# Kernel tuning notes

Measured on AMD Instinct MI355X. Metric: run time of the kernel, lower is better.

Reference implementation:

```python
import jax, jax.numpy as jnp
from jax import lax
import numpy as np

FEA = 256
NHEADS = 8
GROUPS = 32
SCALE = 1.0 / np.sqrt(FEA // NHEADS)  # 1/sqrt(qkv_dim//nheads)


def conv2d(x, w, b=None, pad=0, groups=1):
    out = lax.conv_general_dilated(
        x, w, (1, 1), [(pad, pad), (pad, pad)],
        dimension_numbers=("NCHW", "OIHW", "NCHW"),
        feature_group_count=groups)
    return out if b is None else out + b[None, :, None, None]


def group_norm(x, w, b, groups=GROUPS, eps=1e-5):
    B, C, H, W = x.shape
    xg = x.reshape(B, groups, C // groups, H, W)
    m = xg.mean(axis=(2, 3, 4), keepdims=True)
    v = xg.var(axis=(2, 3, 4), keepdims=True)
    xg = (xg - m) * lax.rsqrt(v + eps)
    return xg.reshape(B, C, H, W) * w[None, :, None, None] + b[None, :, None, None]


def l2norm(x, eps=1e-12):  # F.normalize over channel dim
    n = jnp.sqrt(jnp.sum(x * x, axis=1, keepdims=True))
    return x / jnp.maximum(n, eps)


def attn_op(q, k, v):
    b, c, xf, yf = q.shape
    sp = lambda t: t.reshape(b, NHEADS, c // NHEADS, xf * yf)
    q, k, v = sp(q), sp(k), sp(v)
    sim = jnp.einsum("bhjn,bhkn->bhjk", q, k) * SCALE  # channel attention, [b,h,c/h,c/h]
    sim = jax.nn.softmax(sim, axis=-1)
    out = jnp.einsum("bhjk,bhkn->bhjn", sim, v)
    return out.reshape(b, c, xf, yf)


def freqca(x, gn_w, gn_b, dw_w, pw_w, pw_b, ao_w, ao_b, f1_w, f2_w, f3_w, f3_b):
    H, W = x.shape[-2:]
    x = group_norm(x, gn_w, gn_b)
    qkv = conv2d(conv2d(x, dw_w, pad=1, groups=FEA), pw_w, pw_b)  # depthwise 3x3 then 1x1 -> 3*qkv_dim
    q, k, v = jnp.split(qkv, 3, axis=1)
    q, k, v = l2norm(q), l2norm(k), l2norm(v)
    qf = jnp.fft.rfft2(q, axes=(-2, -1), norm="ortho")
    kf = jnp.fft.rfft2(k, axes=(-2, -1), norm="ortho")
    vf = jnp.fft.rfft2(v, axes=(-2, -1), norm="ortho")
    amp = attn_op(jnp.abs(qf), jnp.abs(kf), jnp.abs(vf))
    phas = attn_op(jnp.angle(qf), jnp.angle(kf), jnp.angle(vf))
    out_c = amp * jnp.cos(phas) + 1j * (amp * jnp.sin(phas))  # torch.polar
    out = jnp.fft.irfft2(out_c, s=(H, W), axes=(-2, -1), norm="ortho")
    attn = conv2d(out, ao_w, ao_b) + x  # attn_res is Identity (fea_dim == dim_out)
    h = jax.nn.silu(conv2d(attn, f1_w, pad=1))
    h = conv2d(h, f2_w, pad=1)
    h = conv2d(h, f3_w, f3_b)
    return h + attn  # DropPath in eval mode = identity


def setup_inputs() -> dict:
    key = jax.random.key(0)
    ks = jax.random.split(key, 12)
    B, C, H, W = 8, FEA, 128, 128
    s = 0.02
    return {
        "x": jax.random.normal(ks[0], (B, C, H, W), jnp.float32),
        "gn_w": jnp.ones((C,), jnp.float32),
        "gn_b": jnp.zeros((C,), jnp.float32),
        "dw_w": jax.random.normal(ks[1], (C, 1, 3, 3), jnp.float32) * s,
        "pw_w": jax.random.normal(ks[2], (3 * C, C, 1, 1), jnp.float32) * s,
        "pw_b": jnp.zeros((3 * C,), jnp.float32),
        "ao_w": jax.random.normal(ks[3], (C, C, 1, 1), jnp.float32) * s,
        "ao_b": jnp.zeros((C,), jnp.float32),
        "f1_w": jax.random.normal(ks[4], (2 * C, C, 3, 3), jnp.float32) * s,
        "f2_w": jax.random.normal(ks[5], (C, 2 * C, 3, 3), jnp.float32) * s,
        "f3_w": jax.random.normal(ks[6], (C, C, 1, 1), jnp.float32) * s,
        "f3_b": jnp.zeros((C,), jnp.float32),
    }


def reference(x, gn_w, gn_b, dw_w, pw_w, pw_b, ao_w, ao_b, f1_w, f2_w, f3_w, f3_b):
    return freqca(x, gn_w, gn_b, dw_w, pw_w, pw_b, ao_w, ao_b, f1_w, f2_w, f3_w, f3_b)
```

## Files before the change

kernel.cpp:

```cpp
#include <hip/hip_runtime.h>
#include <hip/hip_bf16.h>
#include <math.h>


#define TWO_PI_D 6.283185307179586476925286766559
#define ATTN_SCALE 0.17677669529663687f

typedef __attribute__((ext_vector_type(8))) short short8;
typedef __attribute__((ext_vector_type(4))) short short4v;
typedef __attribute__((ext_vector_type(4))) float f32x4;
typedef _Float16 half8v __attribute__((ext_vector_type(8)));

__device__ inline short f2bf(float f) {
    __hip_bfloat16 h = __float2bfloat16(f);
    return *reinterpret_cast<short*>(&h);
}
__device__ inline unsigned short h_bits(_Float16 h) {
    union { _Float16 h; unsigned short u; } c; c.h = h; return c.u;
}

__global__ __launch_bounds__(256) void groupnorm_kernel(
    const float* __restrict__ x, const float* __restrict__ gw,
    const float* __restrict__ gb, float* __restrict__ out, int b0)
{
    int t = threadIdx.x;
    int lb = blockIdx.x >> 5;
    int g  = blockIdx.x & 31;
    size_t src = ((size_t)(b0 + lb) * 32 + g) * 131072;
    size_t dst = (size_t)blockIdx.x * 131072;
    const float* xp = x + src;
    double s = 0.0, ss = 0.0;
    for (int i = t; i < 131072; i += 256) { double v = xp[i]; s += v; ss += v*v; }
    __shared__ double rs[256], rss[256];
    rs[t] = s; rss[t] = ss;
    __syncthreads();
    for (int k = 128; k > 0; k >>= 1) {
        if (t < k) { rs[t] += rs[t+k]; rss[t] += rss[t+k]; }
        __syncthreads();
    }
    __shared__ float smean, sinv;
    if (t == 0) {
        double mean = rs[0] * (1.0/131072.0);
        double var  = rss[0] * (1.0/131072.0) - mean*mean;
        smean = (float)mean;
        sinv  = (float)(1.0 / sqrt(var + 1e-5));
    }
    __syncthreads();
    float mean = smean, inv = sinv;
    for (int i = t; i < 131072; i += 256) {
        int c = (g << 3) + (i >> 14);
        out[dst + i] = (xp[i] - mean) * inv * gw[c] + gb[c];
    }
}

__global__ __launch_bounds__(256) void dwconv_kernel(
    const float* __restrict__ in, const float* __restrict__ w, float* __restrict__ out)
{
    int t = threadIdx.x;
    int bc = blockIdx.x >> 6;
    int y  = ((blockIdx.x & 63) << 1) + (t >> 7);
    int x  = t & 127;
    int c  = bc & 255;
    const float* wp = w + c*9;
    const float* ip = in + ((size_t)bc << 14);
    float acc = 0.f;
    #pragma unroll
    for (int dy = 0; dy < 3; dy++) {
        int yy = y + dy - 1;
        if (yy < 0 || yy > 127) continue;
        const float* row = ip + (yy << 7);
        #pragma unroll
        for (int dx = 0; dx < 3; dx++) {
            int xx = x + dx - 1;
            if (xx >= 0 && xx <= 127) acc += wp[dy*3+dx] * row[xx];
        }
    }
    out[((size_t)bc << 14) + (y << 7) + x] = acc;
}

__global__ __launch_bounds__(256) void wcvtpw_kernel(
    const float* __restrict__ w, _Float16* __restrict__ whi,
    _Float16* __restrict__ wlo, int total)
{
    int i = blockIdx.x * 256 + threadIdx.x;
    if (i >= total) return;
    float v = w[i];
    _Float16 h = (_Float16)v;
    _Float16 l = (_Float16)(v - (float)h);
    whi[i] = h; wlo[i] = l;
}

__global__ __launch_bounds__(256) void convpw_kernel(
    const float* __restrict__ in, const _Float16* __restrict__ whi,
    const _Float16* __restrict__ wlo, const float* __restrict__ bias,
    float* __restrict__ out)
{
    int y      = blockIdx.x;
    int coBase = blockIdx.y << 7;
    int lb     = blockIdx.z;
    int t = threadIdx.x;
    int lane = t & 63;
    int wave = t >> 6;
    int wm = (wave >> 1) << 6;
    int wn = (wave & 1) << 6;
    int lr = lane & 15;
    int kg = (lane >> 4) << 3;

    __shared__ _Float16 Ah[128][40], Al[128][40];
    __shared__ _Float16 Bh[128][40], Bl[128][40];

    f32x4 acc[4][4];
    #pragma unroll
    for (int i = 0; i < 4; i++)
        #pragma unroll
        for (int j = 0; j < 4; j++) acc[i][j] = (f32x4){0.f, 0.f, 0.f, 0.f};

    const float* inrow = in + (((size_t)lb * 256) << 14) + (y << 7);
    for (int ci0 = 0; ci0 < 256; ci0 += 32) {
        __syncthreads();
        #pragma unroll
        for (int u = 0; u < 2; u++) {
            int ii = t + (u << 8);
            int co = ii >> 2, cg = ii & 3;
            *(half8v*)&Ah[co][cg << 3] =
                *(const half8v*)&whi[(size_t)(coBase + co) * 256 + ci0 + (cg << 3)];
            *(half8v*)&Al[co][cg << 3] =
                *(const half8v*)&wlo[(size_t)(coBase + co) * 256 + ci0 + (cg << 3)];
        }
        for (int i = t; i < 2048; i += 256) {
            int px = i & 127, chp = i >> 7;
            int ci = ci0 + (chp << 1);
            float v0 = inrow[((size_t)ci << 14) + px];
            float v1 = inrow[((size_t)(ci + 1) << 14) + px];
            _Float16 h0 = (_Float16)v0, h1 = (_Float16)v1;
            _Float16 l0 = (_Float16)(v0 - (float)h0);
            _Float16 l1 = (_Float16)(v1 - (float)h1);
            unsigned uh = (unsigned)h_bits(h0) | ((unsigned)h_bits(h1) << 16);
            unsigned ul = (unsigned)h_bits(l0) | ((unsigned)h_bits(l1) << 16);
            *(unsigned*)&Bh[px][chp << 1] = uh;
            *(unsigned*)&Bl[px][chp << 1] = ul;
        }
        __syncthreads();
        half8v ah[4], al[4], bh4[4], bl4[4];
        #pragma unroll
        for (int i = 0; i < 4; i++) {
            ah[i] = *(const half8v*)&Ah[wm + i*16 + lr][kg];
            al[i] = *(const half8v*)&Al[wm + i*16 + lr][kg];
        }
        #pragma unroll
        for (int j = 0; j < 4; j++) {
            bh4[j] = *(const half8v*)&Bh[wn + j*16 + lr][kg];
            bl4[j] = *(const half8v*)&Bl[wn + j*16 + lr][kg];
        }
        #pragma unroll
        for (int i = 0; i < 4; i++)
            #pragma unroll
            for (int j = 0; j < 4; j++) {
                acc[i][j] = __builtin_amdgcn_mfma_f32_16x16x32_f16(
                    ah[i], bh4[j], acc[i][j], 0, 0, 0);
                acc[i][j] = __builtin_amdgcn_mfma_f32_16x16x32_f16(
                    ah[i], bl4[j], acc[i][j], 0, 0, 0);
                acc[i][j] = __builtin_amdgcn_mfma_f32_16x16x32_f16(
                    al[i], bh4[j], acc[i][j], 0, 0, 0);
            }
    }

    int pBase = y << 7;
    int mr = (lane >> 4) << 2;
    #pragma unroll
    for (int i = 0; i < 4; i++) {
        int co0 = coBase + wm + i*16 + mr;
        #pragma unroll
        for (int j = 0; j < 4; j++) {
            int px = pBase + wn + j*16 + lr;
            #pragma unroll
            for (int r = 0; r < 4; r++) {
                out[(((size_t)(lb*768 + co0 + r)) << 14) + px] =
                    acc[i][j][r] + bias[co0 + r];
            }
        }
    }
}

__global__ __launch_bounds__(256) void l2inv_kernel(
    const float* __restrict__ qkv, float* __restrict__ invn)
{
    int p  = ((blockIdx.x & 63) << 8) + threadIdx.x;
    int bT = blockIdx.x >> 6;
    int lb = bT / 3, T = bT - 3*lb;
    const float* base = qkv + (((size_t)(lb*768 + T*256)) << 14) + p;
    double ss = 0.0;
    for (int c = 0; c < 256; c++) { double v = base[(size_t)c << 14]; ss += v*v; }
    invn[((size_t)bT << 14) + p] = 1.f / fmaxf((float)sqrt(ss), 1e-12f);
}

__global__ __launch_bounds__(256) void fft_row_kernel(
    const float* __restrict__ qkv, const float* __restrict__ invn,
    float* __restrict__ rre, float* __restrict__ rim, int chunkBase)
{
    int rc  = blockIdx.x;
    int loc = blockIdx.y;
    int gp  = chunkBase + loc;
    int t   = threadIdx.x;
    __shared__ float xs[16][128];
    __shared__ float ex[16][64], od[16][64];
    __shared__ float x0s[16], x64s[16];
    __shared__ float ct[128], st[128];
    if (t < 128) { double s, c; sincos(TWO_PI_D * t / 128.0, &s, &c);
                   st[t] = (float)s; ct[t] = (float)c; }
    int lb = gp / 768, chn = gp - lb*768, T = chn >> 8;
    const float4* src = (const float4*)(qkv + ((size_t)gp << 14) + ((size_t)rc << 11));
    const float4* ivp = (const float4*)(invn + (((size_t)(lb*3 + T)) << 14) + ((size_t)rc << 11));
    float4* xd = (float4*)xs;
    for (int i = t; i < 512; i += 256) {
        float4 v = src[i], w = ivp[i];
        v.x *= w.x; v.y *= w.y; v.z *= w.z; v.w *= w.w;
        xd[i] = v;
    }
    __syncthreads();
    for (int i = t; i < 1008; i += 256) {
        int r = i / 63, w = i - r*63 + 1;
        float a = xs[r][w], b = xs[r][128 - w];
        ex[r][w] = a + b;
        od[r][w] = a - b;
    }
    if (t < 16) { x0s[t] = xs[t][0]; x64s[t] = xs[t][64]; }
    __syncthreads();
    for (int oo = t; oo < 260; oo += 256) {
        int k = oo % 65, rq = oo / 65;
        int r0i = rq << 2;
        float sgn = (k & 1) ? -1.f : 1.f;
        float re0 = x0s[r0i+0] + sgn*x64s[r0i+0];
        float re1 = x0s[r0i+1] + sgn*x64s[r0i+1];
        float re2 = x0s[r0i+2] + sgn*x64s[r0i+2];
        float re3 = x0s[r0i+3] + sgn*x64s[r0i+3];
        float im0 = 0.f, im1 = 0.f, im2 = 0.f, im3 = 0.f;
        int m = k;
        for (int w = 1; w < 64; w++) {
            float cc = ct[m], sn = st[m];
            re0 += ex[r0i+0][w]*cc; im0 -= od[r0i+0][w]*sn;
            re1 += ex[r0i+1][w]*cc; im1 -= od[r0i+1][w]*sn;
            re2 += ex[r0i+2][w]*cc; im2 -= od[r0i+2][w]*sn;
            re3 += ex[r0i+3][w]*cc; im3 -= od[r0i+3][w]*sn;
            m = (m + k) & 127;
        }
        size_t base = ((size_t)loc*128 + rc*16 + (rq << 2))*65 + k;
        rre[base]       = re0*0.0078125f; rim[base]       = im0*0.0078125f;
        rre[base + 65]  = re1*0.0078125f; rim[base + 65]  = im1*0.0078125f;
        rre[base + 130] = re2*0.0078125f; rim[base + 130] = im2*0.0078125f;
        rre[base + 195] = re3*0.0078125f; rim[base + 195] = im3*0.0078125f;
    }
}

__global__ __launch_bounds__(256) void fft_col_kernel(
    const float* __restrict__ rre, const float* __restrict__ rim,
    float* __restrict__ spec, int chunkBase, size_t slotStride)
{
    int kb  = blockIdx.x * 13;
    int loc = blockIdx.y;
    int gp  = chunkBase + loc;
    int t   = threadIdx.x;
    __shared__ float zr[128][14], zi[128][14];
    __shared__ float gr[8][16][14], gi[8][16][14];
    __shared__ float ct[128], st[128];
    if (t < 128) { double s, c; sincos(TWO_PI_D * t / 128.0, &s, &c);
                   st[t] = (float)s; ct[t] = (float)c; }
    for (int i = t; i < 1664; i += 256) {
        int r = i / 13, k = i - r*13;
        size_t si = ((size_t)loc*128 + r)*65 + kb + k;
        zr[r][k] = rre[si];
        zi[r][k] = rim[si];
    }
    __syncthreads();
    for (int i = t; i < 1664; i += 256) {
        int kx = i % 13, rm = i / 13;
        int r0 = rm >> 4, m = rm & 15;
        int step = (m << 3) & 127;
        float gre = 0.f, gim = 0.f;
        int idx = 0;
        for (int r1 = 0; r1 < 16; r1++) {
            float cc = ct[idx], sn = st[idx];
            float a = zr[(r1 << 3) + r0][kx], b = zi[(r1 << 3) + r0][kx];
            gre += a*cc + b*sn;
            gim += b*cc - a*sn;
            idx = (idx + step) & 127;
        }
        gr[r0][m][kx] = gre;
        gi[r0][m][kx] = gim;
    }
    __syncthreads();
    int lb = gp / 768; int chn = gp - lb*768;
    int T = chn >> 8;  int c = chn & 255;
    float* aD = spec + (size_t)(2*T)   * slotStride + ((size_t)(lb*256 + c))*8320;
    float* pD = spec + (size_t)(2*T+1) * slotStride + ((size_t)(lb*256 + c))*8320;
    for (int i = t; i < 1664; i += 256) {
        int kx = i % 13, k1 = i / 13;
        int m = k1 & 15;
        float re = 0.f, im = 0.f;
        int idx = 0;
        for (int r0 = 0; r0 < 8; r0++) {
            float cc = ct[idx], sn = st[idx];
            float a = gr[r0][m][kx], b = gi[r0][m][kx];
            re += a*cc + b*sn;
            im += b*cc - a*sn;
            idx = (idx + k1) & 127;
        }
        int kxv = kb + kx;
        if ((k1 == 0 || k1 == 64) && (kxv == 0 || kxv == 64)) im = 0.f;
        int oi = k1*65 + kxv;
        aD[oi] = sqrtf(re*re + im*im);
        pD[oi] = atan2f(im, re);
    }
}

__global__ __launch_bounds__(256) void attn_sim_kernel(
    const float* __restrict__ qA, const float* __restrict__ kA,
    float* __restrict__ simpart)
{
    int sp = blockIdx.x;
    int bh = blockIdx.y;
    int lb = bh >> 3, h = bh & 7;
    int t = threadIdx.x;
    __shared__ float qs[32][132], ks[32][132];
    const float* qb = qA + ((size_t)(lb*256 + h*32)) * 8320;
    const float* kb = kA + ((size_t)(lb*256 + h*32)) * 8320;
    float acc[4] = {0.f, 0.f, 0.f, 0.f};
    int j0 = t >> 5;
    int kq = t & 31;
    for (int sub = 0; sub < 4; sub++) {
        int n0 = sp*520 + sub*130;
        __syncthreads();
        for (int i = t; i < 4160; i += 256) {
            int j = i / 130, nn = i - j*130;
            qs[j][nn] = qb[(size_t)j*8320 + n0 + nn];
            ks[j][nn] = kb[(size_t)j*8320 + n0 + nn];
        }
        __syncthreads();
        for (int nn = 0; nn < 128; nn += 4) {
            float4 kv = *(const float4*)&ks[kq][nn];
            #pragma unroll
            for (int e = 0; e < 4; e++) {
                float4 qv = *(const float4*)&qs[j0 + e*8][nn];
                acc[e] += qv.x*kv.x + qv.y*kv.y + qv.z*kv.z + qv.w*kv.w;
            }
        }
        {
            float2 kv = *(const float2*)&ks[kq][128];
            #pragma unroll
            for (int e = 0; e < 4; e++) {
                float2 qv = *(const float2*)&qs[j0 + e*8][128];
                acc[e] += qv.x*kv.x + qv.y*kv.y;
            }
        }
    }
    float* dst = simpart + ((size_t)bh*16 + sp) * 1024;
    dst[t]       = acc[0];
    dst[t + 256] = acc[1];
    dst[t + 512] = acc[2];
    dst[t + 768] = acc[3];
}

__global__ __launch_bounds__(256) void attn_out_kernel(
    const float* __restrict__ simpart, const float* __restrict__ vA,
    float* __restrict__ outA)
{
    int nb = blockIdx.x << 8;
    int bh = blockIdx.y;
    int lb = bh >> 3, h = bh & 7;
    int t = threadIdx.x;
    __shared__ float sim[32][32];
    for (int e = t; e < 1024; e += 256) {
        float s = 0.f;
        const float* pp = simpart + (size_t)bh*16384 + e;
        #pragma unroll
        for (int sp = 0; sp < 16; sp++) s += pp[sp*1024];
        sim[e >> 5][e & 31] = s * ATTN_SCALE;
    }
    __syncthreads();
    if (t < 32) {
        float m = -1e30f;
        for (int k = 0; k < 32; k++) m = fmaxf(m, sim[t][k]);
        float s = 0.f;
        for (int k = 0; k < 32; k++) s += expf(sim[t][k] - m);
        float inv = 1.f / s;
        for (int k = 0; k < 32; k++) sim[t][k] = expf(sim[t][k] - m) * inv;
    }
    __syncthreads();
    int n = nb + t;
    if (n >= 8320) return;
    const float* vb = vA + ((size_t)(lb*256 + h*32)) * 8320 + n;
    float vv[32];
    #pragma unroll
    for (int k = 0; k < 32; k++) vv[k] = vb[(size_t)k * 8320];
    float* ob = outA + ((size_t)(lb*256 + h*32)) * 8320 + n;
    for (int j = 0; j < 32; j++) {
        float o = 0.f;
        #pragma unroll
        for (int k = 0; k < 32; k++) o += sim[j][k] * vv[k];
        ob[(size_t)j * 8320] = o;
    }
}

__global__ __launch_bounds__(256) void ifft_col_kernel(
    const float* __restrict__ ampo, const float* __restrict__ pho,
    float* __restrict__ tre, float* __restrict__ tim)
{
    int kb    = blockIdx.x * 13;
    int plane = blockIdx.y;
    int t     = threadIdx.x;
    __shared__ float zr[128][14], zi[128][14];
    __shared__ float gr[8][16][14], gi[8][16][14];
    __shared__ float ct[128], st[128];
    if (t < 128) { double s, c; sincos(TWO_PI_D * t / 128.0, &s, &c);
                   st[t] = (float)s; ct[t] = (float)c; }
    const float* ab = ampo + (size_t)plane * 8320;
    const float* pb = pho  + (size_t)plane * 8320;
    for (int i = t; i < 1664; i += 256) {
        int k1 = i / 13, k = i - k1*13;
        float a = ab[k1*65 + kb + k];
        float p = pb[k1*65 + kb + k];
        float sp, cp; sincosf(p, &sp, &cp);
        zr[k1][k] = a * cp;
        zi[k1][k] = a * sp;
    }
    __syncthreads();
    for (int i = t; i < 1664; i += 256) {
        int kx = i % 13, rm = i / 13;
        int r0 = rm >> 4, m = rm & 15;
        int step = (m << 3) & 127;
        float gre = 0.f, gim = 0.f;
        int idx = 0;
        for (int r1 = 0; r1 < 16; r1++) {
            float cc = ct[idx], sn = st[idx];
            float a = zr[(r1 << 3) + r0][kx], b = zi[(r1 << 3) + r0][kx];
            gre += a*cc - b*sn;
            gim += a*sn + b*cc;
            idx = (idx + step) & 127;
        }
        gr[r0][m][kx] = gre;
        gi[r0][m][kx] = gim;
    }
    __syncthreads();
    for (int i = t; i < 1664; i += 256) {
        int kx = i % 13, y = i / 13;
        int m = y & 15;
        float re = 0.f, im = 0.f;
        int idx = 0;
        for (int r0 = 0; r0 < 8; r0++) {
            float cc = ct[idx], sn = st[idx];
            float a = gr[r0][m][kx], b = gi[r0][m][kx];
            re += a*cc - b*sn;
            im += a*sn + b*cc;
            idx = (idx + y) & 127;
        }
        size_t oi = ((size_t)plane*128 + y)*65 + kb + kx;
        tre[oi] = re;
        tim[oi] = im;
    }
}

__global__ __launch_bounds__(256) void ifft_row_kernel(
    const float* __restrict__ tre, const float* __restrict__ tim,
    float* __restrict__ spat)
{
    int rc    = blockIdx.x;
    int plane = blockIdx.y;
    int t     = threadIdx.x;
    __shared__ float tr[16][66], ti[16][66];
    __shared__ float ct[128], st[128];
    if (t < 128) { double s, c; sincos(TWO_PI_D * t / 128.0, &s, &c);
                   st[t] = (float)s; ct[t] = (float)c; }
    for (int i = t; i < 1040; i += 256) {
        int r = i / 65, k = i - r*65;
        size_t si = ((size_t)plane*128 + rc*16 + r)*65 + k;
        float sc = (k >= 1 && k < 64) ? 2.f : 1.f;
        tr[r][k] = tre[si] * sc;
        ti[r][k] = tim[si] * sc;
    }
    __syncthreads();
    for (int oo = t; oo < 260; oo += 256) {
        int x = oo % 65, rq = oo / 65;
        int r0i = rq << 2;
        float C0 = tr[r0i+0][0], C1 = tr[r0i+1][0], C2 = tr[r0i+2][0], C3 = tr[r0i+3][0];
        float S0 = 0.f, S1 = 0.f, S2 = 0.f, S3 = 0.f;
        int m = x;
        for (int k = 1; k <= 64; k++) {
            float cc = ct[m], sn = st[m];
            C0 += tr[r0i+0][k]*cc; S0 += ti[r0i+0][k]*sn;
            C1 += tr[r0i+1][k]*cc; S1 += ti[r0i+1][k]*sn;
            C2 += tr[r0i+2][k]*cc; S2 += ti[r0i+2][k]*sn;
            C3 += tr[r0i+3][k]*cc; S3 += ti[r0i+3][k]*sn;
            m = (m + x) & 127;
        }
        size_t ob = ((size_t)plane << 14) + ((rc*16 + r0i) << 7);
        spat[ob + x]       = (C0 - S0)*0.0078125f;
        spat[ob + 128 + x] = (C1 - S1)*0.0078125f;
        spat[ob + 256 + x] = (C2 - S2)*0.0078125f;
        spat[ob + 384 + x] = (C3 - S3)*0.0078125f;
        if (x >= 1 && x <= 63) {
            int xm = 128 - x;
            spat[ob + xm]       = (C0 + S0)*0.0078125f;
            spat[ob + 128 + xm] = (C1 + S1)*0.0078125f;
            spat[ob + 256 + xm] = (C2 + S2)*0.0078125f;
            spat[ob + 384 + xm] = (C3 + S3)*0.0078125f;
        }
    }
}

__global__ __launch_bounds__(256) void wcvt_kernel(
    const float* __restrict__ w, short* __restrict__ wbf,
    int Cout, int Cin, int RR)
{
    int i = blockIdx.x * 256 + threadIdx.x;
    int total = Cout * Cin * RR;
    if (i >= total) return;
    int rr = i % RR;
    int ci = (i / RR) % Cin;
    int co = i / (RR * Cin);
    wbf[((size_t)rr * Cout + co) * Cin + ci] = f2bf(w[i]);
}

__global__ __launch_bounds__(256) void convmf2_kernel(
    const float* __restrict__ in, const short* __restrict__ wbf,
    const float* __restrict__ bias, const float* __restrict__ res,
    float* __restrict__ out, short* __restrict__ out_t,
    int Cin, int Cout, int act, int in_b0, int res_b0, int out_b0)
{
    int y      = blockIdx.x;
    int coBase = blockIdx.y << 7;
    int lb = blockIdx.z;
    int t = threadIdx.x;
    int lane = t & 63;
    int wave = t >> 6;
    int wm = (wave >> 1) << 6;
    int wn = (wave & 1) << 6;

    __shared__ short As[128][40];
    __shared__ short Bs[128][40];

    f32x4 acc[4][4];
    #pragma unroll
    for (int i = 0; i < 4; i++)
        #pragma unroll
        for (int j = 0; j < 4; j++) acc[i][j] = (f32x4){0.f, 0.f, 0.f, 0.f};

    const size_t inb = ((size_t)(in_b0 + lb) * Cin) << 14;
    int lr = lane & 15;
    int kg = (lane >> 4) << 3;

    const float* inrow = in + inb + (y << 7);
    const short* wslice = wbf + (size_t)coBase * Cin;
    for (int ci0 = 0; ci0 < Cin; ci0 += 32) {
        __syncthreads();
        #pragma unroll
        for (int u = 0; u < 2; u++) {
            int ii = t + (u << 8);
            int co = ii >> 2, cg = ii & 3;
            *(short8*)&As[co][cg << 3] =
                *(const short8*)&wslice[(size_t)co * Cin + ci0 + (cg << 3)];
        }
        for (int i = t; i < 2048; i += 256) {
            int px = i & 127, chp = i >> 7;
            int ci = ci0 + (chp << 1);
            float v0 = inrow[((size_t)ci << 14) + px];
            float v1 = inrow[((size_t)(ci + 1) << 14) + px];
            unsigned u2 = (unsigned)(unsigned short)f2bf(v0)
                        | ((unsigned)(unsigned short)f2bf(v1) << 16);
            *(unsigned*)&Bs[px][chp << 1] = u2;
        }
        __syncthreads();
        short8 af[4], bf[4];
        #pragma unroll
        for (int i = 0; i < 4; i++)
            af[i] = *(const short8*)&As[wm + i*16 + lr][kg];
        #pragma unroll
        for (int j = 0; j < 4; j++)
            bf[j] = *(const short8*)&Bs[wn + j*16 + lr][kg];
        #pragma unroll
        for (int i = 0; i < 4; i++)
            #pragma unroll
            for (int j = 0; j < 4; j++)
                acc[i][j] = __builtin_amdgcn_mfma_f32_16x16x32_bf16(
                    af[i], bf[j], acc[i][j], 0, 0, 0);
    }

    int pBase = y << 7;
    int mr = (lane >> 4) << 2;
    #pragma unroll
    for (int i = 0; i < 4; i++) {
        int co0 = coBase + wm + i*16 + mr;
        #pragma unroll
        for (int j = 0; j < 4; j++) {
            int px = pBase + wn + j*16 + lr;
            float v[4];
            #pragma unroll
            for (int r = 0; r < 4; r++) {
                float vv = acc[i][j][r] + (bias ? bias[co0 + r] : 0.f);
                if (act == 1) vv = vv / (1.f + expf(-vv));
                if (res) vv += res[(((size_t)(res_b0 + lb) * Cout + co0 + r) << 14) + px];
                v[r] = vv;
            }
            if (out) {
                #pragma unroll
                for (int r = 0; r < 4; r++)
                    out[(((size_t)(out_b0 + lb) * Cout + co0 + r) << 14) + px] = v[r];
            }
            if (out_t) {
                short4v s4 = { f2bf(v[0]), f2bf(v[1]), f2bf(v[2]), f2bf(v[3]) };
                *(short4v*)&out_t[((size_t)(lb*16384 + px)) * Cout + co0] = s4;
            }
        }
    }
}

template<int R>
__global__ __launch_bounds__(256) void convmf3_kernel(
    const short* __restrict__ in_t, const short* __restrict__ wbf,
    const float* __restrict__ bias, const float* __restrict__ res,
    float* __restrict__ out, short* __restrict__ out_t,
    int Cin, int Cout, int act, int res_b0, int out_b0)
{
    int y      = blockIdx.x;
    int coBase = blockIdx.y << 7;
    int lb = blockIdx.z;
    int t = threadIdx.x;
    int lane = t & 63;
    int wave = t >> 6;
    int wm = (wave >> 1) << 6;
    int wn = (wave & 1) << 6;
    int lr = lane & 15;
    int kg = (lane >> 4) << 3;

    f32x4 acc[4][4];
    #pragma unroll
    for (int i = 0; i < 4; i++)
        #pragma unroll
        for (int j = 0; j < 4; j++) acc[i][j] = (f32x4){0.f, 0.f, 0.f, 0.f};

    const short* inb = in_t + (((size_t)lb << 14)) * Cin;
    const short8 zero8 = {0,0,0,0,0,0,0,0};

    for (int rr = 0; rr < R*R; rr++) {
        int dy = (R == 3) ? (rr / 3) : 0;
        int dx = (R == 3) ? (rr - dy*3) : 0;
        int yy = (R == 3) ? (y + dy - 1) : y;
        if (R == 3 && (yy < 0 || yy > 127)) continue;
        const short* wsl  = wbf + ((size_t)rr * Cout + coBase) * Cin;
        const short* brow = inb + ((size_t)(yy << 7)) * Cin;
        for (int ci0 = 0; ci0 < Cin; ci0 += 32) {
            short8 af[4], bf[4];
            #pragma unroll
            for (int i = 0; i < 4; i++)
                af[i] = *(const short8*)&wsl[(size_t)(wm + i*16 + lr) * Cin + ci0 + kg];
            #pragma unroll
            for (int j = 0; j < 4; j++) {
                int pxl = wn + j*16 + lr;
                int xx = (R == 3) ? (pxl + dx - 1) : pxl;
                if (R == 3 && (xx < 0 || xx > 127)) bf[j] = zero8;
                else bf[j] = *(const short8*)&brow[(size_t)xx * Cin + ci0 + kg];
            }
            #pragma unroll
            for (int i = 0; i < 4; i++)
                #pragma unroll
                for (int j = 0; j < 4; j++)
                    acc[i][j] = __builtin_amdgcn_mfma_f32_16x16x32_bf16(
                        af[i], bf[j], acc[i][j], 0, 0, 0);
        }
    }

    int pBase = y << 7;
    int mr = (lane >> 4) << 2;
    #pragma unroll
    for (int i = 0; i < 4; i++) {
        int co0 = coBase + wm + i*16 + mr;
        #pragma unroll
        for (int j = 0; j < 4; j++) {
            int px = pBase + wn + j*16 + lr;
            float v[4];
            #pragma unroll
            for (int r = 0; r < 4; r++) {
                float vv = acc[i][j][r] + (bias ? bias[co0 + r] : 0.f);
                if (act == 1) vv = vv / (1.f + expf(-vv));
                if (res) vv += res[(((size_t)(res_b0 + lb) * Cout + co0 + r) << 14) + px];
                v[r] = vv;
            }
            if (out) {
                #pragma unroll
                for (int r = 0; r < 4; r++)
                    out[(((size_t)(out_b0 + lb) * Cout + co0 + r) << 14) + px] = v[r];
            }
            if (out_t) {
                short4v s4 = { f2bf(v[0]), f2bf(v[1]), f2bf(v[2]), f2bf(v[3]) };
                *(short4v*)&out_t[((size_t)(lb*16384 + px)) * Cout + co0] = s4;
            }
        }
    }
}

extern "C" void kernel_launch(void* const* d_in, const int* in_sizes, int n_in,
                              void* d_out, int out_size, void* d_ws, size_t ws_size,
                              hipStream_t stream) {
    (void)in_sizes; (void)n_in; (void)out_size;
    const float* x    = (const float*)d_in[0];
    const float* gn_w = (const float*)d_in[1];
    const float* gn_b = (const float*)d_in[2];
    const float* dw_w = (const float*)d_in[3];
    const float* pw_w = (const float*)d_in[4];
    const float* pw_b = (const float*)d_in[5];
    const float* ao_w = (const float*)d_in[6];
    const float* ao_b = (const float*)d_in[7];
    const float* f1_w = (const float*)d_in[8];
    const float* f2_w = (const float*)d_in[9];
    const float* f3_w = (const float*)d_in[10];
    const float* f3_b = (const float*)d_in[11];
    float* outp = (float*)d_out;

    const size_t F_QKV  = 12582912;
    const size_t F_SLOT = 2129920;
    const size_t F_SPEC = 6 * F_SLOT;
    const size_t F_XN   = 4194304;
    const size_t F_E    = 4259840;
    const size_t F_SIMP = 262144;
    const size_t F_TOT  = F_QKV + F_SPEC + F_XN + F_E + F_SIMP;
    const size_t F_WB   = 1441792;

    int NB = 0;
    for (int cand : {8, 4, 2, 1}) {
        if (((size_t)cand * F_TOT + F_WB) * 4 <= ws_size) { NB = cand; break; }
    }
    if (NB == 0) return;

    float* wsf  = (float*)d_ws;
    float* qkv  = wsf;
    short* abuf = (short*)wsf;
    short* h1t  = (short*)(wsf + (size_t)NB * 2097152);
    short* h2t  = (short*)(wsf + (size_t)NB * 6291456);
    float* spec = wsf + (size_t)NB * F_QKV;
    size_t ss   = (size_t)NB * F_SLOT;
    float* tre  = spec + 2*ss;
    float* tim  = spec + 3*ss;
    float* spat = spec + 4*ss;
    float* xn   = spec + 6*ss;
    float* ebuf = xn + (size_t)NB * F_XN;
    float* dw   = ebuf;
    float* rre  = ebuf;
    float* rim  = ebuf + (size_t)NB * 2129920;
    float* simpf = ebuf + (size_t)NB * F_E;
    float* invn  = simpf;
    float* simp  = simpf;
    short* wb    = (short*)(wsf + (size_t)NB * F_TOT);
    short* wb_ao = wb;
    short* wb_f1 = wb + 65536;
    short* wb_f2 = wb + 1245184;
    short* wb_f3 = wb + 2424832;
    _Float16* wb_pw_hi = (_Float16*)(wb + 2490368);
    _Float16* wb_pw_lo = (_Float16*)(wb + 2686976);

    wcvt_kernel<<<256,  256, 0, stream>>>(ao_w, wb_ao, 256, 256, 1);
    wcvt_kernel<<<4608, 256, 0, stream>>>(f1_w, wb_f1, 512, 256, 9);
    wcvt_kernel<<<4608, 256, 0, stream>>>(f2_w, wb_f2, 256, 512, 9);
    wcvt_kernel<<<256,  256, 0, stream>>>(f3_w, wb_f3, 256, 256, 1);
    wcvtpw_kernel<<<768, 256, 0, stream>>>(pw_w, wb_pw_hi, wb_pw_lo, 196608);

    const int passes = 8 / NB;
    for (int p = 0; p < passes; p++) {
        int b0 = p * NB;
        groupnorm_kernel<<<NB*32, 256, 0, stream>>>(x, gn_w, gn_b, xn, b0);
        dwconv_kernel<<<NB*256*64, 256, 0, stream>>>(xn, dw_w, dw);
        convpw_kernel<<<dim3(128, 6, NB), 256, 0, stream>>>(
            dw, wb_pw_hi, wb_pw_lo, pw_b, qkv);
        l2inv_kernel<<<NB*3*64, 256, 0, stream>>>(qkv, invn);
        for (int chunk = 0; chunk < 3; chunk++) {
            fft_row_kernel<<<dim3(8, NB*256), 256, 0, stream>>>(
                qkv, invn, rre, rim, chunk*NB*256);
            fft_col_kernel<<<dim3(5, NB*256), 256, 0, stream>>>(
                rre, rim, spec, chunk*NB*256, ss);
        }
        attn_sim_kernel<<<dim3(16, NB*8), 256, 0, stream>>>(spec + 0*ss, spec + 2*ss, simp);
        attn_out_kernel<<<dim3(33, NB*8), 256, 0, stream>>>(simp, spec + 4*ss, spec + 0*ss);
        attn_sim_kernel<<<dim3(16, NB*8), 256, 0, stream>>>(spec + 1*ss, spec + 3*ss, simp);
        attn_out_kernel<<<dim3(33, NB*8), 256, 0, stream>>>(simp, spec + 5*ss, spec + 1*ss);
        ifft_col_kernel<<<dim3(5, NB*256), 256, 0, stream>>>(spec + 0*ss, spec + 1*ss,
                                                             tre, tim);
        ifft_row_kernel<<<dim3(8, NB*256), 256, 0, stream>>>(tre, tim, spat);
        convmf2_kernel<<<dim3(128, 2, NB), 256, 0, stream>>>(
            spat, wb_ao, ao_b, xn, outp, abuf, 256, 256, 0, 0, 0, b0);
        convmf3_kernel<3><<<dim3(128, 4, NB), 256, 0, stream>>>(
            abuf, wb_f1, nullptr, nullptr, nullptr, h1t, 256, 512, 1, 0, 0);
        convmf3_kernel<3><<<dim3(128, 2, NB), 256, 0, stream>>>(
            h1t, wb_f2, nullptr, nullptr, nullptr, h2t, 512, 256, 0, 0, 0);
        convmf3_kernel<1><<<dim3(128, 2, NB), 256, 0, stream>>>(
            h2t, wb_f3, f3_b, outp, outp, nullptr, 256, 256, 0, b0, b0);
    }
}
```

Measured before the change: 7.023 ms.

## Compute row DFT as fp16 split-precision MFMA matmul against precomputed twiddles

Replaces the scalar even/odd row DFT kernel with an MFMA-based kernel that multiplies each 128x128 normalized channel image by a precomputed 128x160 twiddle matrix (cos/sin bins, scaled). Inputs and twiddles are split into hi/lo fp16 pairs and three MFMAs per tile approximate fp32 precision. Twiddles are built once per call into extra workspace. This moves the dominant row-transform arithmetic from VALU loops to matrix cores, at the cost of redundant full-length DFT work (no even/odd symmetry) and some precision risk from the fp16 split.

```diff
diff --git a/kernel.cpp b/kernel.cpp
--- a/kernel.cpp
+++ b/kernel.cpp
@@ -90,6 +90,20 @@
     whi[i] = h; wlo[i] = l;
 }
 
+__global__ __launch_bounds__(256) void twcvt_kernel(
+    _Float16* __restrict__ twh, _Float16* __restrict__ twl)
+{
+    int i = blockIdx.x * 256 + threadIdx.x;
+    if (i >= 20480) return;
+    int bin = i >> 7, w = i & 127;
+    double v = 0.0;
+    if (bin < 65) v = cos(TWO_PI_D * ((bin * w) & 127) / 128.0) * 0.0078125;
+    else if (bin < 130) v = -sin(TWO_PI_D * (((bin - 65) * w) & 127) / 128.0) * 0.0078125;
+    _Float16 h = (_Float16)v;
+    twh[i] = h;
+    twl[i] = (_Float16)((float)v - (float)h);
+}
+
 __global__ __launch_bounds__(256) void convpw_kernel(
     const float* __restrict__ in, const _Float16* __restrict__ whi,
     const _Float16* __restrict__ wlo, const float* __restrict__ bias,
@@ -194,61 +208,96 @@
     invn[((size_t)bT << 14) + p] = 1.f / fmaxf((float)sqrt(ss), 1e-12f);
 }
 
-__global__ __launch_bounds__(256) void fft_row_kernel(
+__global__ __launch_bounds__(256) void fftrow_mfma_kernel(
     const float* __restrict__ qkv, const float* __restrict__ invn,
+    const _Float16* __restrict__ twh, const _Float16* __restrict__ twl,
     float* __restrict__ rre, float* __restrict__ rim, int chunkBase)
 {
-    int rc  = blockIdx.x;
-    int loc = blockIdx.y;
+    int loc = blockIdx.x;
     int gp  = chunkBase + loc;
-    int t   = threadIdx.x;
-    __shared__ float xs[16][128];
-    __shared__ float ex[16][64], od[16][64];
-    __shared__ float x0s[16], x64s[16];
-    __shared__ float ct[128], st[128];
-    if (t < 128) { double s, c; sincos(TWO_PI_D * t / 128.0, &s, &c);
-                   st[t] = (float)s; ct[t] = (float)c; }
+    int t = threadIdx.x;
+    int lane = t & 63;
+    int wave = t >> 6;
+    int wm  = (wave >> 1) << 6;
+    int wnn = (wave & 1) * 80;
+    int lr = lane & 15;
+    int kq = (lane >> 4) << 3;
+
+    __shared__ _Float16 Xh[128][68], Xl[128][68];
+
     int lb = gp / 768, chn = gp - lb*768, T = chn >> 8;
-    const float4* src = (const float4*)(qkv + ((size_t)gp << 14) + ((size_t)rc << 11));
-    const float4* ivp = (const float4*)(invn + (((size_t)(lb*3 + T)) << 14) + ((size_t)rc << 11));
-    float4* xd = (float4*)xs;
-    for (int i = t; i < 512; i += 256) {
-        float4 v = src[i], w = ivp[i];
-        v.x *= w.x; v.y *= w.y; v.z *= w.z; v.w *= w.w;
-        xd[i] = v;
-    }
-    __syncthreads();
-    for (int i = t; i < 1008; i += 256) {
-        int r = i / 63, w = i - r*63 + 1;
-        float a = xs[r][w], b = xs[r][128 - w];
-        ex[r][w] = a + b;
-        od[r][w] = a - b;
-    }
-    if (t < 16) { x0s[t] = xs[t][0]; x64s[t] = xs[t][64]; }
-    __syncthreads();
-    for (int oo = t; oo < 260; oo += 256) {
-        int k = oo % 65, rq = oo / 65;
-        int r0i = rq << 2;
-        float sgn = (k & 1) ? -1.f : 1.f;
-        float re0 = x0s[r0i+0] + sgn*x64s[r0i+0];
-        float re1 = x0s[r0i+1] + sgn*x64s[r0i+1];
-        float re2 = x0s[r0i+2] + sgn*x64s[r0i+2];
-        float re3 = x0s[r0i+3] + sgn*x64s[r0i+3];
-        float im0 = 0.f, im1 = 0.f, im2 = 0.f, im3 = 0.f;
-        int m = k;
-        for (int w = 1; w < 64; w++) {
-            float cc = ct[m], sn = st[m];
-            re0 += ex[r0i+0][w]*cc; im0 -= od[r0i+0][w]*sn;
-            re1 += ex[r0i+1][w]*cc; im1 -= od[r0i+1][w]*sn;
-            re2 += ex[r0i+2][w]*cc; im2 -= od[r0i+2][w]*sn;
-            re3 += ex[r0i+3][w]*cc; im3 -= od[r0i+3][w]*sn;
-            m = (m + k) & 127;
-        }
-        size_t base = ((size_t)loc*128 + rc*16 + (rq << 2))*65 + k;
-        rre[base]       = re0*0.0078125f; rim[base]       = im0*0.0078125f;
-        rre[base + 65]  = re1*0.0078125f; rim[base + 65]  = im1*0.0078125f;
-        rre[base + 130] = re2*0.0078125f; rim[base + 130] = im2*0.0078125f;
-        rre[base + 195] = re3*0.0078125f; rim[base + 195] = im3*0.0078125f;
+    const float4* src = (const float4*)(qkv + ((size_t)gp << 14));
+    const float4* ivp = (const float4*)(invn + (((size_t)(lb*3 + T)) << 14));
+
+    f32x4 acc[4][5];
+    #pragma unroll
+    for (int i = 0; i < 4; i++)
+        #pragma unroll
+        for (int j = 0; j < 5; j++) acc[i][j] = (f32x4){0.f, 0.f, 0.f, 0.f};
+
+    for (int half = 0; half < 2; half++) {
+        __syncthreads();
+        for (int i = t; i < 2048; i += 256) {
+            int r = i >> 4, q4 = i & 15;
+            int gi = (r << 5) + (half << 4) + q4;
+            float4 v = src[gi], w = ivp[gi];
+            v.x *= w.x; v.y *= w.y; v.z *= w.z; v.w *= w.w;
+            int cl = q4 << 2;
+            _Float16 h0 = (_Float16)v.x, h1 = (_Float16)v.y;
+            _Float16 h2 = (_Float16)v.z, h3 = (_Float16)v.w;
+            Xh[r][cl+0] = h0; Xh[r][cl+1] = h1; Xh[r][cl+2] = h2; Xh[r][cl+3] = h3;
+            Xl[r][cl+0] = (_Float16)(v.x - (float)h0);
+            Xl[r][cl+1] = (_Float16)(v.y - (float)h1);
+            Xl[r][cl+2] = (_Float16)(v.z - (float)h2);
+            Xl[r][cl+3] = (_Float16)(v.w - (float)h3);
+        }
+        __syncthreads();
+        #pragma unroll
+        for (int ks = 0; ks < 2; ks++) {
+            int k0 = (ks << 5) + kq;
+            int kg = (half << 6) + k0;
+            half8v ah[4], al[4], bh[5], bl[5];
+            #pragma unroll
+            for (int i = 0; i < 4; i++) {
+                ah[i] = *(const half8v*)&Xh[wm + i*16 + lr][k0];
+                al[i] = *(const half8v*)&Xl[wm + i*16 + lr][k0];
+            }
+            #pragma unroll
+            for (int j = 0; j < 5; j++) {
+                int bin = wnn + j*16 + lr;
+                bh[j] = *(const half8v*)&twh[(size_t)bin * 128 + kg];
+                bl[j] = *(const half8v*)&twl[(size_t)bin * 128 + kg];
+            }
+            #pragma unroll
+            for (int i = 0; i < 4; i++)
+                #pragma unroll
+                for (int j = 0; j < 5; j++) {
+                    acc[i][j] = __builtin_amdgcn_mfma_f32_16x16x32_f16(
+                        ah[i], bh[j], acc[i][j], 0, 0, 0);
+                    acc[i][j] = __builtin_amdgcn_mfma_f32_16x16x32_f16(
+                        al[i], bh[j], acc[i][j], 0, 0, 0);
+                    acc[i][j] = __builtin_amdgcn_mfma_f32_16x16x32_f16(
+                        ah[i], bl[j], acc[i][j], 0, 0, 0);
+                }
+        }
+    }
+
+    int mr = (lane >> 4) << 2;
+    #pragma unroll
+    for (int i = 0; i < 4; i++) {
+        #pragma unroll
+        for (int j = 0; j < 5; j++) {
+            int bin = wnn + j*16 + lr;
+            if (bin < 130) {
+                float* dst = (bin < 65) ? rre : rim;
+                int bb = (bin < 65) ? bin : bin - 65;
+                #pragma unroll
+                for (int r = 0; r < 4; r++) {
+                    int row = wm + i*16 + mr + r;
+                    dst[((size_t)loc*128 + row)*65 + bb] = acc[i][j][r];
+                }
+            }
+        }
     }
 }
 
@@ -722,7 +771,7 @@
     const size_t F_E    = 4259840;
     const size_t F_SIMP = 262144;
     const size_t F_TOT  = F_QKV + F_SPEC + F_XN + F_E + F_SIMP;
-    const size_t F_WB   = 1441792;
+    const size_t F_WB   = 1462272;
 
     int NB = 0;
     for (int cand : {8, 4, 2, 1}) {
@@ -755,12 +804,15 @@
     short* wb_f3 = wb + 2424832;
     _Float16* wb_pw_hi = (_Float16*)(wb + 2490368);
     _Float16* wb_pw_lo = (_Float16*)(wb + 2686976);
+    _Float16* wb_tw_hi = (_Float16*)(wb + 2883584);
+    _Float16* wb_tw_lo = (_Float16*)(wb + 2904064);
 
     wcvt_kernel<<<256,  256, 0, stream>>>(ao_w, wb_ao, 256, 256, 1);
     wcvt_kernel<<<4608, 256, 0, stream>>>(f1_w, wb_f1, 512, 256, 9);
     wcvt_kernel<<<4608, 256, 0, stream>>>(f2_w, wb_f2, 256, 512, 9);
     wcvt_kernel<<<256,  256, 0, stream>>>(f3_w, wb_f3, 256, 256, 1);
     wcvtpw_kernel<<<768, 256, 0, stream>>>(pw_w, wb_pw_hi, wb_pw_lo, 196608);
+    twcvt_kernel<<<80, 256, 0, stream>>>(wb_tw_hi, wb_tw_lo);
 
     const int passes = 8 / NB;
     for (int p = 0; p < passes; p++) {
@@ -771,8 +823,8 @@
             dw, wb_pw_hi, wb_pw_lo, pw_b, qkv);
         l2inv_kernel<<<NB*3*64, 256, 0, stream>>>(qkv, invn);
         for (int chunk = 0; chunk < 3; chunk++) {
-            fft_row_kernel<<<dim3(8, NB*256), 256, 0, stream>>>(
-                qkv, invn, rre, rim, chunk*NB*256);
+            fftrow_mfma_kernel<<<NB*256, 256, 0, stream>>>(
+                qkv, invn, wb_tw_hi, wb_tw_lo, rre, rim, chunk*NB*256);
             fft_col_kernel<<<dim3(5, NB*256), 256, 0, stream>>>(
                 rre, rim, spec, chunk*NB*256, ss);
         }
```

After: 6.460 ms. 1.09x faster.
